# Kernel optimization log

Hardware: AMD Instinct MI355X
Metric: run time of the kernel (lower is better)

Reference implementation:

```python
import jax, jax.numpy as jnp
import numpy as np
from jax import lax

DIM = 4096
N_HEADS = 32
N_KV_HEADS = 8
HEAD_DIM = DIM // N_HEADS  # 128
N_REP = N_HEADS // N_KV_HEADS  # 4
B, S = 1, 2048
ROPE_THETA = 10000.0
NEG_INF = -1e9


def setup_inputs() -> dict:
    key = jax.random.key(0)
    ks = jax.random.split(key, 6)
    scale = 1.0 / np.sqrt(DIM)
    x = jax.random.normal(ks[0], (B, S, DIM), dtype=jnp.float32)
    wq = jax.random.normal(ks[1], (DIM, DIM), dtype=jnp.float32) * scale
    wk = jax.random.normal(ks[2], (N_KV_HEADS * HEAD_DIM, DIM), dtype=jnp.float32) * scale
    wv = jax.random.normal(ks[3], (N_KV_HEADS * HEAD_DIM, DIM), dtype=jnp.float32) * scale
    wo = jax.random.normal(ks[4], (DIM, DIM), dtype=jnp.float32) * scale
    # Llama rotary frequencies: freqs_cis[t, i] = exp(i * t * theta^(-2i/d))
    inv_freq = 1.0 / (ROPE_THETA ** (np.arange(0, HEAD_DIM, 2, dtype=np.float32) / HEAD_DIM))
    angles = np.outer(np.arange(S, dtype=np.float32), inv_freq)  # [S, HEAD_DIM//2]
    freqs_cos = jnp.asarray(np.cos(angles), dtype=jnp.float32)
    freqs_sin = jnp.asarray(np.sin(angles), dtype=jnp.float32)
    cache_k = jnp.zeros((B, S, N_KV_HEADS, HEAD_DIM), dtype=jnp.float32)
    cache_v = jnp.zeros((B, S, N_KV_HEADS, HEAD_DIM), dtype=jnp.float32)
    # causal mask added to scores (broadcasts over [B, H, S, S])
    mask = jnp.where(np.triu(np.ones((S, S), dtype=bool), k=1), NEG_INF, 0.0).astype(jnp.float32)
    return {"x": x, "wq": wq, "wk": wk, "wv": wv, "wo": wo,
            "freqs_cos": freqs_cos, "freqs_sin": freqs_sin,
            "cache_k": cache_k, "cache_v": cache_v, "mask": mask,
            "start_pos": 0}


def _apply_rotary(t, cos, sin):
    # t: [B, S, H, HEAD_DIM]; cos/sin: [S, HEAD_DIM//2]
    b, s, h, d = t.shape
    tr = t.reshape(b, s, h, d // 2, 2)
    a, bb = tr[..., 0], tr[..., 1]  # real / imag of consecutive pairs
    c = cos[None, :, None, :]
    sn = sin[None, :, None, :]
    out_r = a * c - bb * sn
    out_i = a * sn + bb * c
    return jnp.stack([out_r, out_i], axis=-1).reshape(b, s, h, d)


def reference(x, wq, wk, wv, wo, freqs_cos, freqs_sin, cache_k, cache_v, mask, start_pos):
    bsz, seqlen, _ = x.shape
    xq = jnp.einsum('bsd,od->bso', x, wq).reshape(bsz, seqlen, N_HEADS, HEAD_DIM)
    xk = jnp.einsum('bsd,od->bso', x, wk).reshape(bsz, seqlen, N_KV_HEADS, HEAD_DIM)
    xv = jnp.einsum('bsd,od->bso', x, wv).reshape(bsz, seqlen, N_KV_HEADS, HEAD_DIM)
    xq = _apply_rotary(xq, freqs_cos, freqs_sin)
    xk = _apply_rotary(xk, freqs_cos, freqs_sin)
    # KV-cache append
    cache_k = lax.dynamic_update_slice(cache_k, xk, (0, start_pos, 0, 0))
    cache_v = lax.dynamic_update_slice(cache_v, xv, (0, start_pos, 0, 0))
    kv_len = start_pos + seqlen
    keys = cache_k[:, :kv_len]    # [B, KVLEN, KV, HD]
    values = cache_v[:, :kv_len]
    # GQA: repeat_interleave over kv heads
    keys = jnp.repeat(keys, N_REP, axis=2)      # [B, KVLEN, H, HD]
    values = jnp.repeat(values, N_REP, axis=2)
    q = xq.transpose(0, 2, 1, 3)       # [B, H, S, HD]
    k = keys.transpose(0, 2, 1, 3)     # [B, H, KVLEN, HD]
    v = values.transpose(0, 2, 1, 3)
    scores = jnp.einsum('bhqd,bhkd->bhqk', q, k) / np.sqrt(HEAD_DIM)
    scores = scores + mask[None, None, :, :]
    probs = jax.nn.softmax(scores.astype(jnp.float32), axis=-1).astype(q.dtype)
    out = jnp.einsum('bhqk,bhkd->bhqd', probs, v)
    out = out.transpose(0, 2, 1, 3).reshape(bsz, seqlen, -1)
    return jnp.einsum('bso,do->bsd', out, wo)
```

## Files before the change

kernel.cpp:

```cpp
#include <hip/hip_runtime.h>
#include <hip/hip_bf16.h>

typedef unsigned short u16;
typedef unsigned int u32;
typedef __bf16 bf16x8 __attribute__((ext_vector_type(8)));
typedef float f32x4 __attribute__((ext_vector_type(4)));
typedef u32 u32x4 __attribute__((ext_vector_type(4)));

#define QKV_LD 6144
#define KOFF 4096
#define VOFF 5120
#define HD 128
#define DIM 4096

__device__ __forceinline__ u16 f2bf(float f) {
  union { __hip_bfloat16 h; u16 u; } c;
  c.h = __float2bfloat16(f);
  return c.u;
}
__device__ __forceinline__ float bf2f(u16 u) {
  union { u16 u; __hip_bfloat16 h; } c;
  c.u = u;
  return __bfloat162float(c.h);
}

typedef __attribute__((address_space(1))) const u32 gas_u32;
typedef __attribute__((address_space(3))) u32 las_u32;
__device__ __forceinline__ void async16(const u16* g, u16* l) {
  __builtin_amdgcn_global_load_lds((gas_u32*)g, (las_u32*)l, 16, 0, 0);
}

__device__ __forceinline__ void store_out(u16* p, float v) { *p = f2bf(v); }
__device__ __forceinline__ void store_out(float* p, float v) { *p = v; }

__global__ __launch_bounds__(256) void cvt_kernel(const float* __restrict__ src,
                                                  u16* __restrict__ dst, int n8) {
  int i = blockIdx.x * 256 + threadIdx.x;
  if (i >= n8) return;
  const f32x4* s4 = (const f32x4*)src;
  f32x4 a = s4[2 * i], b = s4[2 * i + 1];
  u32x4 o;
  o[0] = (u32)f2bf(a[0]) | ((u32)f2bf(a[1]) << 16);
  o[1] = (u32)f2bf(a[2]) | ((u32)f2bf(a[3]) << 16);
  o[2] = (u32)f2bf(b[0]) | ((u32)f2bf(b[1]) << 16);
  o[3] = (u32)f2bf(b[2]) | ((u32)f2bf(b[3]) << 16);
  ((u32x4*)dst)[i] = o;
}

#define BAR8 __builtin_amdgcn_s_barrier()
#define VMC(n) asm volatile("s_waitcnt vmcnt(" #n ")" ::: "memory")

#define LDA8(buf, half, arr)                                                     \
  _Pragma("unroll") for (int mi = 0; mi < 4; ++mi) {                             \
    const int r_ = wm * 64 + mi * 16 + l16;                                      \
    const u16* p_ = &lds[buf][half][r_ * 64];                                    \
    _Pragma("unroll") for (int ks = 0; ks < 2; ++ks)                             \
      arr[mi][ks] = *(const bf16x8*)(p_ + (((ks * 4 + quad) ^ (r_ & 7)) << 3));  \
  }

#define LDB8(buf, half, arr)                                                     \
  _Pragma("unroll") for (int ni = 0; ni < 2; ++ni) {                             \
    const int r_ = wn * 32 + ni * 16 + l16;                                      \
    const u16* p_ = &lds[buf][2 + (half)][r_ * 64];                              \
    _Pragma("unroll") for (int ks = 0; ks < 2; ++ks)                             \
      arr[ni][ks] = *(const bf16x8*)(p_ + (((ks * 4 + quad) ^ (r_ & 7)) << 3));  \
  }

#define MMA8(qm, qn, af, bf)                                                       \
  __builtin_amdgcn_s_setprio(1);                                                   \
  _Pragma("unroll") for (int mi = 0; mi < 4; ++mi)                                 \
  _Pragma("unroll") for (int ni = 0; ni < 2; ++ni)                                 \
  _Pragma("unroll") for (int ks = 0; ks < 2; ++ks)                                 \
    acc[(qm) * 4 + mi][(qn) * 2 + ni] = __builtin_amdgcn_mfma_f32_16x16x32_bf16(   \
        af[mi][ks], bf[ni][ks], acc[(qm) * 4 + mi][(qn) * 2 + ni], 0, 0, 0);       \
  __builtin_amdgcn_s_setprio(0);

template <typename OutT>
__global__ __launch_bounds__(512, 2) void gemm_nt8(const u16* __restrict__ A,
                                                   const u16* __restrict__ B,
                                                   OutT* __restrict__ C,
                                                   int N, int K, int MT) {
  __shared__ u16 lds[2][4][128 * 64];
  const int tid = threadIdx.x;
  const int wave = tid >> 6;
  const int lane = tid & 63;
  const int quad = lane >> 4;
  const int l16 = lane & 15;
  const int wm = wave >> 2;
  const int wn = wave & 3;

  const int nwg = gridDim.x;
  const int bid = blockIdx.x;
  const int qq = nwg >> 3, rr8 = nwg & 7, xcd = bid & 7, off = bid >> 3;
  const int wg = (xcd < rr8 ? xcd * (qq + 1) : rr8 * (qq + 1) + (xcd - rr8) * qq) + off;
  const int bm = wg % MT;
  const int bn = wg / MT;

  const int NIT = K >> 7;

  const int srow = (wave << 3) + (lane >> 3);
  const int sgran = (lane & 7) ^ ((lane >> 3) & 7);
  const u16* Abase = A + (size_t)(bm * 256 + srow) * K + sgran * 8;
  const u16* Bbase = B + (size_t)(bn * 256 + srow) * K + sgran * 8;

  auto stage = [&](const u16* base, int h, int kt, u16* slot) {
    const u16* g = base + (size_t)(h * 128) * K + kt * 64;
    u16* s = slot + wave * (8 * 64);
    async16(g, s);
    async16(g + (size_t)64 * K, s + 64 * 64);
  };

  f32x4 acc[8][4];
#pragma unroll
  for (int i = 0; i < 8; ++i)
#pragma unroll
    for (int j = 0; j < 4; ++j) {
      f32x4 z = {0.f, 0.f, 0.f, 0.f};
      acc[i][j] = z;
    }

  stage(Abase, 0, 0, &lds[0][0][0]);
  stage(Bbase, 0, 0, &lds[0][2][0]);
  stage(Bbase, 1, 0, &lds[0][3][0]);
  stage(Abase, 1, 0, &lds[0][1][0]);
  stage(Abase, 0, 1, &lds[1][0][0]);
  stage(Bbase, 0, 1, &lds[1][2][0]);
  stage(Bbase, 1, 1, &lds[1][3][0]);
  VMC(6);
  BAR8;

  bf16x8 a0[4][2], a1[4][2], b0[2][2], b1[2][2];
  for (int it = 0; it < NIT; ++it) {
    const int t2 = 2 * it + 2, t3 = 2 * it + 3;
    const bool more = (it + 1 < NIT);

    LDA8(0, 0, a0);
    LDB8(0, 0, b0);
    stage(Abase, 1, 2 * it + 1, &lds[1][1][0]);
    BAR8;
    MMA8(0, 0, a0, b0);
    BAR8;
    LDB8(0, 1, b1);
    if (more) stage(Abase, 0, t2, &lds[0][0][0]);
    BAR8;
    MMA8(0, 1, a0, b1);
    BAR8;
    LDA8(0, 1, a1);
    if (more) stage(Bbase, 0, t2, &lds[0][2][0]);
    BAR8;
    MMA8(1, 1, a1, b1);
    BAR8;
    if (more) stage(Bbase, 1, t2, &lds[0][3][0]);
    BAR8;
    MMA8(1, 0, a1, b0);
    if (more) { VMC(6); } else { VMC(0); }
    BAR8;
    LDA8(1, 0, a0);
    LDB8(1, 0, b0);
    if (more) stage(Abase, 1, t2, &lds[0][1][0]);
    BAR8;
    MMA8(0, 0, a0, b0);
    BAR8;
    LDB8(1, 1, b1);
    if (more) stage(Abase, 0, t3, &lds[1][0][0]);
    BAR8;
    MMA8(0, 1, a0, b1);
    BAR8;
    LDA8(1, 1, a1);
    if (more) stage(Bbase, 0, t3, &lds[1][2][0]);
    BAR8;
    MMA8(1, 1, a1, b1);
    BAR8;
    if (more) stage(Bbase, 1, t3, &lds[1][3][0]);
    BAR8;
    MMA8(1, 0, a1, b0);
    if (more) { VMC(6); } else { VMC(0); }
    BAR8;
  }

#pragma unroll
  for (int qm = 0; qm < 2; ++qm)
#pragma unroll
    for (int mi = 0; mi < 4; ++mi) {
      int row = bm * 256 + qm * 128 + wm * 64 + mi * 16 + quad * 4;
#pragma unroll
      for (int qn = 0; qn < 2; ++qn)
#pragma unroll
        for (int ni = 0; ni < 2; ++ni) {
          int col = bn * 256 + qn * 128 + wn * 32 + ni * 16 + l16;
#pragma unroll
          for (int r = 0; r < 4; ++r)
            store_out(&C[(size_t)(row + r) * N + col], acc[qm * 4 + mi][qn * 2 + ni][r]);
        }
    }
}

#define LDAW(buf, arr)                                                               \
  _Pragma("unroll") for (int qm_ = 0; qm_ < 2; ++qm_)                                \
  _Pragma("unroll") for (int mi = 0; mi < 2; ++mi) {                                 \
    const int r_ = qm_ * 64 + wm * 32 + mi * 16 + l16;                               \
    const u16* p_ = &lds[buf][0][r_ * 64];                                           \
    _Pragma("unroll") for (int ks = 0; ks < 2; ++ks)                                 \
      arr[qm_][mi][ks] = *(const bf16x8*)(p_ + (((ks * 4 + quad) ^ (r_ & 7)) << 3)); \
  }

#define LDBW(buf, h, arr)                                                        \
  _Pragma("unroll") for (int ni = 0; ni < 2; ++ni) {                             \
    const int r_ = wn * 32 + ni * 16 + l16;                                      \
    const u16* p_ = &lds[buf][1 + (h)][r_ * 64];                                 \
    _Pragma("unroll") for (int ks = 0; ks < 2; ++ks)                             \
      arr[ni][ks] = *(const bf16x8*)(p_ + (((ks * 4 + quad) ^ (r_ & 7)) << 3));  \
  }

#define MMAW(qm, qn, af, bf)                                                       \
  __builtin_amdgcn_s_setprio(1);                                                   \
  _Pragma("unroll") for (int mi = 0; mi < 2; ++mi)                                 \
  _Pragma("unroll") for (int ni = 0; ni < 2; ++ni)                                 \
  _Pragma("unroll") for (int ks = 0; ks < 2; ++ks)                                 \
    acc[(qm) * 2 + mi][(qn) * 2 + ni] = __builtin_amdgcn_mfma_f32_16x16x32_bf16(   \
        af[qm][mi][ks], bf[ni][ks], acc[(qm) * 2 + mi][(qn) * 2 + ni], 0, 0, 0);   \
  __builtin_amdgcn_s_setprio(0);

template <typename OutT>
__global__ __launch_bounds__(512, 2) void gemm_nt8w(const u16* __restrict__ A,
                                                    const u16* __restrict__ B,
                                                    OutT* __restrict__ C,
                                                    int N, int K, int MT) {
  __shared__ u16 lds[2][3][128 * 64];
  const int tid = threadIdx.x;
  const int wave = tid >> 6;
  const int lane = tid & 63;
  const int quad = lane >> 4;
  const int l16 = lane & 15;
  const int wm = wave >> 2;
  const int wn = wave & 3;

  const int nwg = gridDim.x;
  const int bid = blockIdx.x;
  const int qq = nwg >> 3, rr8 = nwg & 7, xcd = bid & 7, off = bid >> 3;
  const int wg = (xcd < rr8 ? xcd * (qq + 1) : rr8 * (qq + 1) + (xcd - rr8) * qq) + off;
  const int bm = wg % MT;
  const int bn = wg / MT;

  const int NIT = K >> 7;

  const int srow = (wave << 3) + (lane >> 3);
  const int sgran = (lane & 7) ^ ((lane >> 3) & 7);
  const u16* Abase = A + (size_t)(bm * 128 + srow) * K + sgran * 8;
  const u16* Bbase = B + (size_t)(bn * 256 + srow) * K + sgran * 8;

  auto stageA = [&](int buf, int kt) {
    const u16* g = Abase + (size_t)kt * 64;
    u16* s = &lds[buf][0][0] + wave * (8 * 64);
    async16(g, s);
    async16(g + (size_t)64 * K, s + 64 * 64);
  };
  auto stageB = [&](int buf, int h, int kt) {
    const u16* g = Bbase + (size_t)(h * 128) * K + kt * 64;
    u16* s = &lds[buf][1 + h][0] + wave * (8 * 64);
    async16(g, s);
    async16(g + (size_t)64 * K, s + 64 * 64);
  };

  f32x4 acc[4][4];
#pragma unroll
  for (int i = 0; i < 4; ++i)
#pragma unroll
    for (int j = 0; j < 4; ++j) {
      f32x4 z = {0.f, 0.f, 0.f, 0.f};
      acc[i][j] = z;
    }

  stageA(0, 0); stageB(0, 0, 0); stageB(0, 1, 0);
  stageA(1, 1); stageB(1, 0, 1); stageB(1, 1, 1);
  VMC(6);
  BAR8;

  bf16x8 a[2][2][2], b0f[2][2], b1f[2][2];
  for (int it = 0; it < NIT; ++it) {
    const int t2 = 2 * it + 2, t3 = 2 * it + 3;
    const bool more = (it + 1 < NIT);

    LDAW(0, a);
    LDBW(0, 0, b0f);
    BAR8;
    MMAW(0, 0, a, b0f);
    BAR8;
    LDBW(0, 1, b1f);
    if (more) stageB(0, 0, t2);
    BAR8;
    MMAW(0, 1, a, b1f);
    BAR8;
    if (more) stageA(0, t2);
    BAR8;
    MMAW(1, 1, a, b1f);
    BAR8;
    if (more) stageB(0, 1, t2);
    BAR8;
    MMAW(1, 0, a, b0f);
    if (more) { VMC(6); } else { VMC(0); }
    BAR8;
    LDAW(1, a);
    LDBW(1, 0, b0f);
    BAR8;
    MMAW(0, 0, a, b0f);
    BAR8;
    LDBW(1, 1, b1f);
    if (more) stageB(1, 0, t3);
    BAR8;
    MMAW(0, 1, a, b1f);
    BAR8;
    if (more) stageA(1, t3);
    BAR8;
    MMAW(1, 1, a, b1f);
    BAR8;
    if (more) stageB(1, 1, t3);
    BAR8;
    MMAW(1, 0, a, b0f);
    if (more) { VMC(6); } else { VMC(0); }
    BAR8;
  }

#pragma unroll
  for (int qm = 0; qm < 2; ++qm)
#pragma unroll
    for (int mi = 0; mi < 2; ++mi) {
      int row = bm * 128 + qm * 64 + wm * 32 + mi * 16 + quad * 4;
#pragma unroll
      for (int qn = 0; qn < 2; ++qn)
#pragma unroll
        for (int ni = 0; ni < 2; ++ni) {
          int col = bn * 256 + qn * 128 + wn * 32 + ni * 16 + l16;
#pragma unroll
          for (int r = 0; r < 4; ++r)
            store_out(&C[(size_t)(row + r) * N + col], acc[qm * 2 + mi][qn * 2 + ni][r]);
        }
    }
}

__global__ __launch_bounds__(256) void rope_kernel(u16* qkv, const float* __restrict__ fcos,
                                                   const float* __restrict__ fsin) {
  int idx = blockIdx.x * 256 + threadIdx.x;
  int row, colbase, fi;
  if (idx < 2048 * 2048) {
    row = idx >> 11;
    int pi = idx & 2047;
    fi = pi & 63;
    colbase = (pi >> 6) * 128 + fi * 2;
  } else {
    int j = idx - 2048 * 2048;
    row = j >> 9;
    int pj = j & 511;
    fi = pj & 63;
    colbase = KOFF + (pj >> 6) * 128 + fi * 2;
  }
  float c = fcos[row * 64 + fi], s = fsin[row * 64 + fi];
  u32* p = (u32*)(qkv + (size_t)row * QKV_LD + colbase);
  u32 v = *p;
  float a = bf2f((u16)(v & 0xffffu));
  float b = bf2f((u16)(v >> 16));
  float xr = a * c - b * s;
  float xi = a * s + b * c;
  *p = (u32)f2bf(xr) | ((u32)f2bf(xi) << 16);
}

__global__ __launch_bounds__(256) void vtrans_kernel(const u16* __restrict__ qkv,
                                                     u16* __restrict__ vt) {
  __shared__ u16 Ls[64 * 72];
  const int tid = threadIdx.x;
  const int st = blockIdx.x, dt = blockIdx.y, kvh = blockIdx.z;
#pragma unroll
  for (int t = 0; t < 2; ++t) {
    int g = t * 256 + tid;
    int s = g >> 3, c = g & 7;
    u32x4 v = *(const u32x4*)(qkv + (size_t)(st * 64 + s) * QKV_LD + VOFF + kvh * HD + dt * 64 + c * 8);
    *(u32x4*)&Ls[s * 72 + c * 8] = v;
  }
  __syncthreads();
#pragma unroll
  for (int t = 0; t < 2; ++t) {
    int g = t * 256 + tid;
    int d = g >> 3, c2 = g & 7;
    u32x4 o;
#pragma unroll
    for (int j = 0; j < 4; ++j) {
      u16 lo = Ls[(c2 * 8 + 2 * j) * 72 + d];
      u16 hi = Ls[(c2 * 8 + 2 * j + 1) * 72 + d];
      o[j] = (u32)lo | ((u32)hi << 16);
    }
    *(u32x4*)(vt + (size_t)(kvh * HD + dt * 64 + d) * 2048 + st * 64 + c2 * 8) = o;
  }
}

__global__ __launch_bounds__(256, 2) void flash_kernel(const u16* __restrict__ qkv,
                                                       const u16* __restrict__ vt,
                                                       u16* __restrict__ attnb) {
  __shared__ u16 Kl[2][64 * 128];
  __shared__ u16 VtL[2][128 * 64];
  __shared__ u16 Pl[4][16 * 72];
  const int tid = threadIdx.x;
  const int wave = tid >> 6;
  const int lane = tid & 63;
  const int quad = lane >> 4;
  const int l16 = lane & 15;
  const int lid = blockIdx.x;
  const int h = lid & 31;
  const int z = lid >> 5;
  const int qt = (z < 8) ? z : 23 - z;
  const int kvh = h >> 2;
  const float scale = 0.08838834764831845f;
  const int nkt = 2 * qt + 2;

  const int krow_l = (lane >> 4);
  const int kcol_l = (lane & 15);
  const int vd_l = (lane >> 3);
  const int vc = (lane & 7) ^ ((lane >> 3) & 7);

  const u16* kbase = qkv + (size_t)KOFF + kvh * HD;
  const u16* vbase = vt + (size_t)kvh * HD * 2048;

  bf16x8 qf[2][4];
#pragma unroll
  for (int mi = 0; mi < 2; ++mi) {
    const u16* qp = qkv + (size_t)(qt * 128 + wave * 32 + mi * 16 + l16) * QKV_LD + h * HD + quad * 8;
#pragma unroll
    for (int ks = 0; ks < 4; ++ks) qf[mi][ks] = *(const bf16x8*)(qp + ks * 32);
  }

  f32x4 o[2][8];
#pragma unroll
  for (int mi = 0; mi < 2; ++mi)
#pragma unroll
    for (int i = 0; i < 8; ++i) { f32x4 zz = {0.f, 0.f, 0.f, 0.f}; o[mi][i] = zz; }
  float lacc[2] = {0.f, 0.f};

#pragma unroll
  for (int t = 0; t < 4; ++t) {
    int i = wave * 4 + t;
    int row = i * 4 + krow_l;
    int c = kcol_l ^ (row & 15);
    async16(kbase + (size_t)row * QKV_LD + c * 8, &Kl[0][i * 512]);
  }
#pragma unroll
  for (int t = 0; t < 4; ++t) {
    int i = wave * 4 + t;
    int d = i * 8 + vd_l;
    async16(vbase + (size_t)d * 2048 + vc * 8, &VtL[0][i * 512]);
  }

  for (int kt = 0; kt < nkt; ++kt) {
    const int cur = kt & 1;
    __syncthreads();

    f32x4 s4[2][4];
#pragma unroll
    for (int mi = 0; mi < 2; ++mi)
#pragma unroll
      for (int nb = 0; nb < 4; ++nb) { f32x4 zz = {0.f, 0.f, 0.f, 0.f}; s4[mi][nb] = zz; }
#pragma unroll
    for (int nb = 0; nb < 4; ++nb) {
#pragma unroll
      for (int ks = 0; ks < 4; ++ks) {
        int rr = nb * 16 + l16;
        int cc = ((ks * 4 + quad) ^ l16) * 8;
        bf16x8 kf = *(const bf16x8*)&Kl[cur][rr * 128 + cc];
        s4[0][nb] = __builtin_amdgcn_mfma_f32_16x16x32_bf16(qf[0][ks], kf, s4[0][nb], 0, 0, 0);
        s4[1][nb] = __builtin_amdgcn_mfma_f32_16x16x32_bf16(qf[1][ks], kf, s4[1][nb], 0, 0, 0);
      }
    }

    bf16x8 vb[16];
#pragma unroll
    for (int db = 0; db < 8; ++db) {
      int dd = db * 16 + l16;
#pragma unroll
      for (int ks2 = 0; ks2 < 2; ++ks2) {
        int c = (ks2 * 4 + quad) ^ (dd & 7);
        vb[db * 2 + ks2] = *(const bf16x8*)&VtL[cur][dd * 64 + c * 8];
      }
    }

    float p[2][4][4];
    const bool diag = (kt >= 2 * qt);
    if (diag) {
#pragma unroll
      for (int mi = 0; mi < 2; ++mi)
#pragma unroll
        for (int nb = 0; nb < 4; ++nb) {
          int col = kt * 64 + nb * 16 + l16;
#pragma unroll
          for (int r = 0; r < 4; ++r) {
            int row = qt * 128 + wave * 32 + mi * 16 + quad * 4 + r;
            p[mi][nb][r] = (col > row) ? 0.f : __expf(s4[mi][nb][r] * scale);
          }
        }
    } else {
#pragma unroll
      for (int mi = 0; mi < 2; ++mi)
#pragma unroll
        for (int nb = 0; nb < 4; ++nb)
#pragma unroll
          for (int r = 0; r < 4; ++r)
            p[mi][nb][r] = __expf(s4[mi][nb][r] * scale);
    }

    bf16x8 pa[2][2];
#pragma unroll
    for (int mi = 0; mi < 2; ++mi) {
#pragma unroll
      for (int nb = 0; nb < 4; ++nb)
#pragma unroll
        for (int r = 0; r < 4; ++r)
          Pl[wave][(quad * 4 + r) * 72 + nb * 16 + l16] = f2bf(p[mi][nb][r]);
      __asm__ __volatile__("s_waitcnt lgkmcnt(0)" ::: "memory");
#pragma unroll
      for (int ks2 = 0; ks2 < 2; ++ks2)
        pa[mi][ks2] = *(const bf16x8*)&Pl[wave][l16 * 72 + ks2 * 32 + quad * 8];
    }

#pragma unroll
    for (int mi = 0; mi < 2; ++mi) {
      float sm = 0.f;
#pragma unroll
      for (int ks2 = 0; ks2 < 2; ++ks2)
#pragma unroll
        for (int j = 0; j < 8; ++j) sm += (float)pa[mi][ks2][j];
      sm += __shfl_xor(sm, 16);
      sm += __shfl_xor(sm, 32);
      lacc[mi] += sm;
    }

    if (kt + 1 < nkt) {
      const u16* kb = kbase + (size_t)(kt + 1) * 64 * QKV_LD;
      const u16* vb2 = vbase + (kt + 1) * 64;
#pragma unroll
      for (int t = 0; t < 4; ++t) {
        int i = wave * 4 + t;
        int row = i * 4 + krow_l;
        int c = kcol_l ^ (row & 15);
        async16(kb + (size_t)row * QKV_LD + c * 8, &Kl[1 - cur][i * 512]);
      }
#pragma unroll
      for (int t = 0; t < 4; ++t) {
        int i = wave * 4 + t;
        int d = i * 8 + vd_l;
        async16(vb2 + (size_t)d * 2048 + vc * 8, &VtL[1 - cur][i * 512]);
      }
    }

#pragma unroll
    for (int mi = 0; mi < 2; ++mi)
#pragma unroll
      for (int db = 0; db < 8; ++db)
#pragma unroll
        for (int ks2 = 0; ks2 < 2; ++ks2)
          o[mi][db] = __builtin_amdgcn_mfma_f32_16x16x32_bf16(pa[mi][ks2], vb[db * 2 + ks2], o[mi][db], 0, 0, 0);
  }

  float* lsh = (float*)&Pl[wave][0];
  if (quad == 0) {
    lsh[l16] = lacc[0];
    lsh[16 + l16] = lacc[1];
  }
  __asm__ __volatile__("s_waitcnt lgkmcnt(0)" ::: "memory");
  __builtin_amdgcn_wave_barrier();
  f32x4 inv[2];
#pragma unroll
  for (int mi = 0; mi < 2; ++mi) {
    f32x4 lv = *(const f32x4*)&lsh[mi * 16 + quad * 4];
#pragma unroll
    for (int r = 0; r < 4; ++r) inv[mi][r] = 1.f / lv[r];
  }
#pragma unroll
  for (int mi = 0; mi < 2; ++mi)
#pragma unroll
    for (int db = 0; db < 8; ++db)
#pragma unroll
      for (int r = 0; r < 4; ++r) {
        int row = qt * 128 + wave * 32 + mi * 16 + quad * 4 + r;
        int col = h * HD + db * 16 + l16;
        attnb[(size_t)row * DIM + col] = f2bf(o[mi][db][r] * inv[mi][r]);
      }
}

extern "C" void kernel_launch(void* const* d_in, const int* in_sizes, int n_in,
                              void* d_out, int out_size, void* d_ws, size_t ws_size,
                              hipStream_t stream) {
  (void)in_sizes; (void)n_in; (void)out_size; (void)ws_size;
  const float* x    = (const float*)d_in[0];
  const float* wq   = (const float*)d_in[1];
  const float* wk   = (const float*)d_in[2];
  const float* wv   = (const float*)d_in[3];
  const float* wo   = (const float*)d_in[4];
  const float* fcos = (const float*)d_in[5];
  const float* fsin = (const float*)d_in[6];
  float* out = (float*)d_out;

  char* ws = (char*)d_ws;
  u16* xb    = (u16*)(ws);
  u16* wqkvb = (u16*)(ws + (size_t)16777216);
  u16* wob   = (u16*)(ws + (size_t)67108864);
  u16* qkv   = (u16*)(ws + (size_t)100663296);
  u16* attnb = (u16*)(ws + (size_t)125829120);
  u16* vtb   = (u16*)(ws);

  cvt_kernel<<<4096, 256, 0, stream>>>(x, xb, 1048576);
  cvt_kernel<<<8192, 256, 0, stream>>>(wq, wqkvb, 2097152);
  cvt_kernel<<<2048, 256, 0, stream>>>(wk, wqkvb + 16777216, 524288);
  cvt_kernel<<<2048, 256, 0, stream>>>(wv, wqkvb + 20971520, 524288);
  cvt_kernel<<<8192, 256, 0, stream>>>(wo, wob, 2097152);

  gemm_nt8<u16><<<dim3(192), 512, 0, stream>>>(xb, wqkvb, qkv, 6144, 4096, 8);
  vtrans_kernel<<<dim3(32, 2, 8), 256, 0, stream>>>(qkv, vtb);
  rope_kernel<<<20480, 256, 0, stream>>>(qkv, fcos, fsin);
  flash_kernel<<<512, 256, 0, stream>>>(qkv, vtb, attnb);
  gemm_nt8w<float><<<dim3(256), 512, 0, stream>>>(attnb, wob, out, 4096, 4096, 16);
}
```

Baseline: 531.5 us.

## Retile QKV GEMM to 128x384 blocks for full CU coverage

The QKV projection GEMM is retiled from 256x256 output tiles (192 workgroups) to 128x384 tiles (256 workgroups), so that on a 256-CU part every CU gets one block instead of leaving a quarter idle. Each wave now computes a 64x96 subtile with a 2x3 MFMA fragment layout, and the LDS staging and pipeline schedule are rearranged so that one A slot and three B slots are staged per k-step. In exchange, the smaller M tile lowers arithmetic intensity per block and the B-slot index math is more complex.

```diff
diff --git a/kernel.cpp b/kernel.cpp
--- a/kernel.cpp
+++ b/kernel.cpp
@@ -50,36 +50,37 @@
 #define BAR8 __builtin_amdgcn_s_barrier()
 #define VMC(n) asm volatile("s_waitcnt vmcnt(" #n ")" ::: "memory")
 
-#define LDA8(buf, half, arr)                                                     \
-  _Pragma("unroll") for (int mi = 0; mi < 4; ++mi) {                             \
-    const int r_ = wm * 64 + mi * 16 + l16;                                      \
-    const u16* p_ = &lds[buf][half][r_ * 64];                                    \
-    _Pragma("unroll") for (int ks = 0; ks < 2; ++ks)                             \
-      arr[mi][ks] = *(const bf16x8*)(p_ + (((ks * 4 + quad) ^ (r_ & 7)) << 3));  \
-  }
-
-#define LDB8(buf, half, arr)                                                     \
-  _Pragma("unroll") for (int ni = 0; ni < 2; ++ni) {                             \
-    const int r_ = wn * 32 + ni * 16 + l16;                                      \
-    const u16* p_ = &lds[buf][2 + (half)][r_ * 64];                              \
-    _Pragma("unroll") for (int ks = 0; ks < 2; ++ks)                             \
-      arr[ni][ks] = *(const bf16x8*)(p_ + (((ks * 4 + quad) ^ (r_ & 7)) << 3));  \
-  }
-
-#define MMA8(qm, qn, af, bf)                                                       \
-  __builtin_amdgcn_s_setprio(1);                                                   \
-  _Pragma("unroll") for (int mi = 0; mi < 4; ++mi)                                 \
-  _Pragma("unroll") for (int ni = 0; ni < 2; ++ni)                                 \
-  _Pragma("unroll") for (int ks = 0; ks < 2; ++ks)                                 \
-    acc[(qm) * 4 + mi][(qn) * 2 + ni] = __builtin_amdgcn_mfma_f32_16x16x32_bf16(   \
-        af[mi][ks], bf[ni][ks], acc[(qm) * 4 + mi][(qn) * 2 + ni], 0, 0, 0);       \
+#define LDAQ(buf, mh, arr)                                                        \
+  _Pragma("unroll") for (int mi = 0; mi < 2; ++mi) {                              \
+    const int r_ = wm * 64 + (mh) * 32 + mi * 16 + l16;                           \
+    const u16* p_ = &lds[buf][0][r_ * 64];                                        \
+    _Pragma("unroll") for (int ks = 0; ks < 2; ++ks)                              \
+      arr[mi][ks] = *(const bf16x8*)(p_ + (((ks * 4 + quad) ^ (r_ & 7)) << 3));   \
+  }
+
+#define LDBQ(buf, nh, arr)                                                        \
+  _Pragma("unroll") for (int ni = 0; ni < 3; ++ni) {                              \
+    const int gr_ = wn * 96 + (nh) * 48 + ni * 16 + l16;                          \
+    const int sl_ = (wn * 96 + (nh) * 48 + ni * 16) >> 7;                         \
+    const u16* p_ = &lds[buf][1 + sl_][(gr_ & 127) * 64];                         \
+    _Pragma("unroll") for (int ks = 0; ks < 2; ++ks)                              \
+      arr[ni][ks] = *(const bf16x8*)(p_ + (((ks * 4 + quad) ^ (gr_ & 7)) << 3));  \
+  }
+
+#define MMAQ(mh, nh, af, bf)                                                      \
+  __builtin_amdgcn_s_setprio(1);                                                  \
+  _Pragma("unroll") for (int mi = 0; mi < 2; ++mi)                                \
+  _Pragma("unroll") for (int ni = 0; ni < 3; ++ni)                                \
+  _Pragma("unroll") for (int ks = 0; ks < 2; ++ks)                                \
+    acc[(mh) * 2 + mi][(nh) * 3 + ni] = __builtin_amdgcn_mfma_f32_16x16x32_bf16(  \
+        af[mi][ks], bf[ni][ks], acc[(mh) * 2 + mi][(nh) * 3 + ni], 0, 0, 0);      \
   __builtin_amdgcn_s_setprio(0);
 
 template <typename OutT>
-__global__ __launch_bounds__(512, 2) void gemm_nt8(const u16* __restrict__ A,
-                                                   const u16* __restrict__ B,
-                                                   OutT* __restrict__ C,
-                                                   int N, int K, int MT) {
+__global__ __launch_bounds__(512, 2) void gemm_nt8q(const u16* __restrict__ A,
+                                                    const u16* __restrict__ B,
+                                                    OutT* __restrict__ C,
+                                                    int N, int K, int MT) {
   __shared__ u16 lds[2][4][128 * 64];
   const int tid = threadIdx.x;
   const int wave = tid >> 6;
@@ -100,97 +101,98 @@
 
   const int srow = (wave << 3) + (lane >> 3);
   const int sgran = (lane & 7) ^ ((lane >> 3) & 7);
-  const u16* Abase = A + (size_t)(bm * 256 + srow) * K + sgran * 8;
-  const u16* Bbase = B + (size_t)(bn * 256 + srow) * K + sgran * 8;
-
-  auto stage = [&](const u16* base, int h, int kt, u16* slot) {
-    const u16* g = base + (size_t)(h * 128) * K + kt * 64;
-    u16* s = slot + wave * (8 * 64);
+  const u16* Abase = A + (size_t)(bm * 128 + srow) * K + sgran * 8;
+  const u16* Bbase = B + (size_t)(bn * 384 + srow) * K + sgran * 8;
+
+  auto stageA = [&](int buf, int kt) {
+    const u16* g = Abase + (size_t)kt * 64;
+    u16* s = &lds[buf][0][0] + wave * (8 * 64);
     async16(g, s);
     async16(g + (size_t)64 * K, s + 64 * 64);
   };
-
-  f32x4 acc[8][4];
-#pragma unroll
-  for (int i = 0; i < 8; ++i)
-#pragma unroll
-    for (int j = 0; j < 4; ++j) {
+  auto stageB = [&](int buf, int j, int kt) {
+    const u16* g = Bbase + (size_t)(j * 128) * K + (size_t)kt * 64;
+    u16* s = &lds[buf][1 + j][0] + wave * (8 * 64);
+    async16(g, s);
+    async16(g + (size_t)64 * K, s + 64 * 64);
+  };
+
+  f32x4 acc[4][6];
+#pragma unroll
+  for (int i = 0; i < 4; ++i)
+#pragma unroll
+    for (int j = 0; j < 6; ++j) {
       f32x4 z = {0.f, 0.f, 0.f, 0.f};
       acc[i][j] = z;
     }
 
-  stage(Abase, 0, 0, &lds[0][0][0]);
-  stage(Bbase, 0, 0, &lds[0][2][0]);
-  stage(Bbase, 1, 0, &lds[0][3][0]);
-  stage(Abase, 1, 0, &lds[0][1][0]);
-  stage(Abase, 0, 1, &lds[1][0][0]);
-  stage(Bbase, 0, 1, &lds[1][2][0]);
-  stage(Bbase, 1, 1, &lds[1][3][0]);
-  VMC(6);
+  stageB(0, 0, 0); stageB(0, 1, 0); stageB(0, 2, 0); stageA(0, 0);
+  stageB(1, 0, 1); stageB(1, 1, 1);
+  VMC(4);
   BAR8;
 
-  bf16x8 a0[4][2], a1[4][2], b0[2][2], b1[2][2];
+  bf16x8 alo[2][2], ahi[2][2], blo[3][2], bhi[3][2];
   for (int it = 0; it < NIT; ++it) {
-    const int t2 = 2 * it + 2, t3 = 2 * it + 3;
+    const int t1 = 2 * it + 1, t2 = 2 * it + 2, t3 = 2 * it + 3;
     const bool more = (it + 1 < NIT);
 
-    LDA8(0, 0, a0);
-    LDB8(0, 0, b0);
-    stage(Abase, 1, 2 * it + 1, &lds[1][1][0]);
-    BAR8;
-    MMA8(0, 0, a0, b0);
-    BAR8;
-    LDB8(0, 1, b1);
-    if (more) stage(Abase, 0, t2, &lds[0][0][0]);
-    BAR8;
-    MMA8(0, 1, a0, b1);
-    BAR8;
-    LDA8(0, 1, a1);
-    if (more) stage(Bbase, 0, t2, &lds[0][2][0]);
-    BAR8;
-    MMA8(1, 1, a1, b1);
-    BAR8;
-    if (more) stage(Bbase, 1, t2, &lds[0][3][0]);
-    BAR8;
-    MMA8(1, 0, a1, b0);
-    if (more) { VMC(6); } else { VMC(0); }
-    BAR8;
-    LDA8(1, 0, a0);
-    LDB8(1, 0, b0);
-    if (more) stage(Abase, 1, t2, &lds[0][1][0]);
-    BAR8;
-    MMA8(0, 0, a0, b0);
-    BAR8;
-    LDB8(1, 1, b1);
-    if (more) stage(Abase, 0, t3, &lds[1][0][0]);
-    BAR8;
-    MMA8(0, 1, a0, b1);
-    BAR8;
-    LDA8(1, 1, a1);
-    if (more) stage(Bbase, 0, t3, &lds[1][2][0]);
-    BAR8;
-    MMA8(1, 1, a1, b1);
-    BAR8;
-    if (more) stage(Bbase, 1, t3, &lds[1][3][0]);
-    BAR8;
-    MMA8(1, 0, a1, b0);
-    if (more) { VMC(6); } else { VMC(0); }
-    BAR8;
-  }
-
-#pragma unroll
-  for (int qm = 0; qm < 2; ++qm)
-#pragma unroll
-    for (int mi = 0; mi < 4; ++mi) {
-      int row = bm * 256 + qm * 128 + wm * 64 + mi * 16 + quad * 4;
-#pragma unroll
-      for (int qn = 0; qn < 2; ++qn)
-#pragma unroll
-        for (int ni = 0; ni < 2; ++ni) {
-          int col = bn * 256 + qn * 128 + wn * 32 + ni * 16 + l16;
+    LDAQ(0, 0, alo);
+    LDBQ(0, 0, blo);
+    stageB(1, 2, t1);
+    BAR8;
+    MMAQ(0, 0, alo, blo);
+    BAR8;
+    LDBQ(0, 1, bhi);
+    stageA(1, t1);
+    BAR8;
+    MMAQ(0, 1, alo, bhi);
+    BAR8;
+    LDAQ(0, 1, ahi);
+    if (more) stageB(0, 0, t2);
+    BAR8;
+    MMAQ(1, 1, ahi, bhi);
+    BAR8;
+    if (more) stageB(0, 1, t2);
+    BAR8;
+    MMAQ(1, 0, ahi, blo);
+    if (more) { VMC(4); } else { VMC(0); }
+    BAR8;
+    LDAQ(1, 0, alo);
+    LDBQ(1, 0, blo);
+    if (more) stageB(0, 2, t2);
+    BAR8;
+    MMAQ(0, 0, alo, blo);
+    BAR8;
+    LDBQ(1, 1, bhi);
+    if (more) stageA(0, t2);
+    BAR8;
+    MMAQ(0, 1, alo, bhi);
+    BAR8;
+    LDAQ(1, 1, ahi);
+    if (more) stageB(1, 0, t3);
+    BAR8;
+    MMAQ(1, 1, ahi, bhi);
+    BAR8;
+    if (more) stageB(1, 1, t3);
+    BAR8;
+    MMAQ(1, 0, ahi, blo);
+    if (more) { VMC(4); } else { VMC(0); }
+    BAR8;
+  }
+
+#pragma unroll
+  for (int mh = 0; mh < 2; ++mh)
+#pragma unroll
+    for (int mi = 0; mi < 2; ++mi) {
+      int row = bm * 128 + wm * 64 + mh * 32 + mi * 16 + quad * 4;
+#pragma unroll
+      for (int nh = 0; nh < 2; ++nh)
+#pragma unroll
+        for (int ni = 0; ni < 3; ++ni) {
+          int col = bn * 384 + wn * 96 + nh * 48 + ni * 16 + l16;
 #pragma unroll
           for (int r = 0; r < 4; ++r)
-            store_out(&C[(size_t)(row + r) * N + col], acc[qm * 4 + mi][qn * 2 + ni][r]);
+            store_out(&C[(size_t)(row + r) * N + col], acc[mh * 2 + mi][nh * 3 + ni][r]);
         }
     }
 }
@@ -610,7 +612,7 @@
   cvt_kernel<<<2048, 256, 0, stream>>>(wv, wqkvb + 20971520, 524288);
   cvt_kernel<<<8192, 256, 0, stream>>>(wo, wob, 2097152);
 
-  gemm_nt8<u16><<<dim3(192), 512, 0, stream>>>(xb, wqkvb, qkv, 6144, 4096, 8);
+  gemm_nt8q<u16><<<dim3(256), 512, 0, stream>>>(xb, wqkvb, qkv, 6144, 4096, 16);
   vtrans_kernel<<<dim3(32, 2, 8), 256, 0, stream>>>(qkv, vtb);
   rope_kernel<<<20480, 256, 0, stream>>>(qkv, fcos, fsin);
   flash_kernel<<<512, 256, 0, stream>>>(qkv, vtb, attnb);
```

New measurement: 523.4 us. Within noise of the previous version (-1.5%).
